# Kernel tuning notes

Measured on AMD Instinct MI355X. Metric: run time of the kernel, lower is better.

## Reference

```python
import jax, jax.numpy as jnp
import numpy as np

EPS_DEPTH = 0.001  # validity threshold from target_points.ge(0.001)
BIG = 1e10         # stands in for masked-out (padded) y points


def setup_inputs() -> dict:
    key = jax.random.key(0)
    k1, k2 = jax.random.split(key)
    L, N, P1 = 4, 4, 257          # n_scales, batch, n_bin_edges (256 bins)
    H, W = 240, 320
    bins = jax.random.uniform(k1, (L, N, P1), dtype=jnp.float32)
    target_depth_maps = jax.random.uniform(k2, (N, H, W), dtype=jnp.float32)
    return {"bins": bins, "target_depth_maps": target_depth_maps}


def _chamfer_1d(centers, y, mask, y_lengths):
    # centers: [N, P] bin centers; y: [N, M] flattened depths; mask: [N, M] valid
    # squared pairwise distances in 1-D: [N, P, M]
    d = (centers[:, :, None] - y[:, None, :]) ** 2
    # x -> y: min over VALID y points, mean over P bin centers
    dx = jnp.where(mask[:, None, :], d, BIG)
    cham_x = dx.min(axis=2).mean(axis=1)                       # [N]
    # y -> x: min over bin centers, sum over valid y / y_length
    dy = jnp.where(mask, d.min(axis=1), 0.0)                   # [N, M]
    cham_y = dy.sum(axis=1) / y_lengths                        # [N]
    return (cham_x + cham_y).mean()  # batch_reduction="mean"


def reference(bins, target_depth_maps):
    N = target_depth_maps.shape[0]
    y = target_depth_maps.reshape(N, -1)                       # [N, M]
    mask = y >= EPS_DEPTH                                      # ragged validity mask
    y_lengths = mask.sum(axis=1).astype(y.dtype)               # [N]
    loss = jnp.zeros((), dtype=y.dtype)
    for bin_edges in bins:  # fixed small loop over scales (multi=True)
        centers = 0.5 * (bin_edges[:, 1:] + bin_edges[:, :-1])  # [N, P]
        loss = loss + _chamfer_1d(centers, y, mask, y_lengths)
    return loss
```

## Files before the change

### kernel.cpp

```cpp
#include <hip/hip_runtime.h>


#define NSCALES 4
#define NBATCH  4
#define NEDGES  257
#define NP      256
#define NM      76800
#define CHUNK   512
#define NCHUNK  (NM / CHUNK)
#define BLOCK   256
#define NCENT   (NSCALES * NP)
#define BIGF    1e10f

__global__ __launch_bounds__(BLOCK) void bcl_init(float* __restrict__ minabs,
                                                  float* __restrict__ sumy,
                                                  unsigned int* __restrict__ cnt) {
    int t = blockIdx.x * blockDim.x + threadIdx.x;
    if (t < NSCALES * NBATCH * NP) minabs[t] = BIGF;
    if (t < NSCALES * NBATCH)      sumy[t]   = 0.0f;
    if (t < NBATCH)                cnt[t]    = 0u;
}

__global__ __launch_bounds__(BLOCK) void bcl_main(const float* __restrict__ bins,
                                                  const float* __restrict__ depth,
                                                  float* __restrict__ minabs,
                                                  float* __restrict__ sumy,
                                                  unsigned int* __restrict__ cnt) {
    __shared__ float sY[CHUNK];
    __shared__ float sC[NCENT];
    __shared__ float redS[BLOCK / 64][NSCALES];
    __shared__ unsigned int redC[BLOCK / 64];

    const int b = blockIdx.x;
    const int n = b / NCHUNK;
    const int chunk = b - n * NCHUNK;
    const int t = threadIdx.x;

    const float* yp = depth + n * NM + chunk * CHUNK;
#pragma unroll
    for (int k = 0; k < CHUNK / BLOCK; ++k) {
        float v = yp[t + k * BLOCK];
        sY[t + k * BLOCK] = (v >= 0.001f) ? v : 3e9f;
    }
#pragma unroll
    for (int k = 0; k < NCENT / BLOCK; ++k) {
        int i = t + k * BLOCK;
        int l = i >> 8;
        int p = i & (NP - 1);
        const float* be = bins + (l * NBATCH + n) * NEDGES + p;
        sC[i] = 0.5f * (be[0] + be[1]);
    }
    __syncthreads();

    float ca[NSCALES], ma[NSCALES];
#pragma unroll
    for (int k = 0; k < NSCALES; ++k) { ca[k] = sC[t + k * BLOCK]; ma[k] = BIGF; }

    const float4* sY4 = (const float4*)sY;
#pragma unroll 2
    for (int q = 0; q < CHUNK / 4; ++q) {
        float4 yv = sY4[q];
#pragma unroll
        for (int k = 0; k < NSCALES; ++k) {
            ma[k] = fminf(ma[k], fabsf(ca[k] - yv.x));
            ma[k] = fminf(ma[k], fabsf(ca[k] - yv.y));
            ma[k] = fminf(ma[k], fabsf(ca[k] - yv.z));
            ma[k] = fminf(ma[k], fabsf(ca[k] - yv.w));
        }
    }
#pragma unroll
    for (int k = 0; k < NSCALES; ++k)
        atomicMin((int*)(minabs + (k * NBATCH + n) * NP + t), __float_as_int(ma[k]));

    float yb0 = sY[t];
    float yb1 = sY[t + BLOCK];
    const bool v0 = yb0 < 2.0f, v1 = yb1 < 2.0f;

    float suml[NSCALES];
    const float4* sC4 = (const float4*)sC;
#pragma unroll
    for (int l = 0; l < NSCALES; ++l) {
        float m0 = BIGF, m1 = BIGF;
#pragma unroll 4
        for (int q = 0; q < NP / 4; ++q) {
            float4 c = sC4[l * (NP / 4) + q];
            m0 = fminf(m0, fabsf(c.x - yb0));  m1 = fminf(m1, fabsf(c.x - yb1));
            m0 = fminf(m0, fabsf(c.y - yb0));  m1 = fminf(m1, fabsf(c.y - yb1));
            m0 = fminf(m0, fabsf(c.z - yb0));  m1 = fminf(m1, fabsf(c.z - yb1));
            m0 = fminf(m0, fabsf(c.w - yb0));  m1 = fminf(m1, fabsf(c.w - yb1));
        }
        float s = 0.0f;
        if (v0) s += m0 * m0;
        if (v1) s += m1 * m1;
        suml[l] = s;
    }
    unsigned int c = (v0 ? 1u : 0u) + (v1 ? 1u : 0u);

#pragma unroll
    for (int off = 32; off; off >>= 1) {
#pragma unroll
        for (int l = 0; l < NSCALES; ++l) suml[l] += __shfl_down(suml[l], off);
        c += __shfl_down(c, off);
    }
    const int wv = t >> 6;
    if ((t & 63) == 0) {
#pragma unroll
        for (int l = 0; l < NSCALES; ++l) redS[wv][l] = suml[l];
        redC[wv] = c;
    }
    __syncthreads();
    if (t < NSCALES) {
        float s = redS[0][t] + redS[1][t] + redS[2][t] + redS[3][t];
        atomicAdd(&sumy[t * NBATCH + n], s);
    }
    if (t == 0) {
        unsigned int cc = redC[0] + redC[1] + redC[2] + redC[3];
        atomicAdd(&cnt[n], cc);
    }
}

__global__ __launch_bounds__(BLOCK) void bcl_final(const float* __restrict__ minabs,
                                                   const float* __restrict__ sumy,
                                                   const unsigned int* __restrict__ cnt,
                                                   float* __restrict__ out) {
    __shared__ float red[BLOCK / 64];
    int t = threadIdx.x;
    float s = 0.0f;
#pragma unroll
    for (int k = 0; k < (NSCALES * NBATCH * NP) / BLOCK; ++k) {
        float m = minabs[t + k * BLOCK];
        s += m * m;
    }
#pragma unroll
    for (int off = 32; off; off >>= 1) s += __shfl_down(s, off);
    if ((t & 63) == 0) red[t >> 6] = s;
    __syncthreads();
    if (t == 0) {
        float S = red[0] + red[1] + red[2] + red[3];
        float lossA = S / (float)NP;
        float lossB = 0.0f;
#pragma unroll
        for (int i = 0; i < NSCALES * NBATCH; ++i)
            lossB += sumy[i] / (float)cnt[i & (NBATCH - 1)];
        out[0] = (lossA + lossB) / (float)NBATCH;
    }
}

extern "C" void kernel_launch(void* const* d_in, const int* in_sizes, int n_in,
                              void* d_out, int out_size, void* d_ws, size_t ws_size,
                              hipStream_t stream) {
    const float* bins  = (const float*)d_in[0];
    const float* depth = (const float*)d_in[1];

    float* minabs = (float*)d_ws;
    float* sumy   = minabs + NSCALES * NBATCH * NP;
    unsigned int* cnt = (unsigned int*)(sumy + NSCALES * NBATCH);

    bcl_init<<<(NSCALES * NBATCH * NP + BLOCK - 1) / BLOCK, BLOCK, 0, stream>>>(minabs, sumy, cnt);
    bcl_main<<<NBATCH * NCHUNK, BLOCK, 0, stream>>>(bins, depth, minabs, sumy, cnt);
    bcl_final<<<1, BLOCK, 0, stream>>>(minabs, sumy, cnt, (float*)d_out);
}
```

Measured before the change: 85.35 us.

## Replace brute-force 1-D chamfer with sorted centers, binary search and interval extrema

A prep kernel computes the bin centers and sorts them with a bitonic sort per (scale, batch). The main kernel then binary-searches each depth value into the sorted centers to get its nearest-center distance. It also records per-interval max and min depth with shared-then-global atomics, so the x->y nearest depth can be recovered in the final kernel by prefix and suffix scans. This removes the O(P*M) brute-force min loops. In exchange it adds a sort, divergent searches and many atomics.

```diff
diff --git a/kernel.cpp b/kernel.cpp
--- a/kernel.cpp
+++ b/kernel.cpp
@@ -9,25 +9,59 @@
 #define CHUNK   512
 #define NCHUNK  (NM / CHUNK)
 #define BLOCK   256
-#define NCENT   (NSCALES * NP)
+#define NLN     (NSCALES * NBATCH)
+#define NIV     (NP + 1)
 #define BIGF    1e10f
-
-__global__ __launch_bounds__(BLOCK) void bcl_init(float* __restrict__ minabs,
-                                                  float* __restrict__ sumy,
-                                                  unsigned int* __restrict__ cnt) {
-    int t = blockIdx.x * blockDim.x + threadIdx.x;
-    if (t < NSCALES * NBATCH * NP) minabs[t] = BIGF;
-    if (t < NSCALES * NBATCH)      sumy[t]   = 0.0f;
-    if (t < NBATCH)                cnt[t]    = 0u;
-}
-
-__global__ __launch_bounds__(BLOCK) void bcl_main(const float* __restrict__ bins,
-                                                  const float* __restrict__ depth,
-                                                  float* __restrict__ minabs,
-                                                  float* __restrict__ sumy,
-                                                  unsigned int* __restrict__ cnt) {
-    __shared__ float sY[CHUNK];
-    __shared__ float sC[NCENT];
+#define IMIN    ((int)0x80000000)
+#define IMAX    0x7fffffff
+
+#define WS_SORTC 0
+#define WS_GA    (WS_SORTC + NLN * NP)
+#define WS_GB    (WS_GA + NLN * NIV)
+#define WS_SUMY  (WS_GB + NLN * NIV)
+#define WS_CNT   (WS_SUMY + NLN)
+
+__global__ __launch_bounds__(BLOCK) void bcl_prep(const float* __restrict__ bins,
+                                                  float* __restrict__ ws) {
+    __shared__ float s[NP];
+    const int b = blockIdx.x;
+    const int t = threadIdx.x;
+    const float* e = bins + b * NEDGES;
+    s[t] = 0.5f * (e[t] + e[t + 1]);
+
+    for (int k = 2; k <= NP; k <<= 1) {
+        for (int j = k >> 1; j > 0; j >>= 1) {
+            __syncthreads();
+            const int ixj = t ^ j;
+            const float a = s[t];
+            const float c = s[ixj];
+            const bool up = ((t & k) == 0);
+            float keep;
+            if (ixj > t) keep = up ? fminf(a, c) : fmaxf(a, c);
+            else         keep = up ? fmaxf(a, c) : fminf(a, c);
+            __syncthreads();
+            s[t] = keep;
+        }
+    }
+    __syncthreads();
+    ws[WS_SORTC + b * NP + t] = s[t];
+
+    int* gA = (int*)ws + WS_GA + b * NIV;
+    int* gB = (int*)ws + WS_GB + b * NIV;
+    gA[t] = IMIN;
+    gB[t] = IMAX;
+    if (t == 0) { gA[NP] = IMIN; gB[NP] = IMAX; }
+    if (b == 0) {
+        if (t < NLN)    ws[WS_SUMY + t] = 0.0f;
+        if (t < NBATCH) ((unsigned int*)ws)[WS_CNT + t] = 0u;
+    }
+}
+
+__global__ __launch_bounds__(BLOCK) void bcl_main(const float* __restrict__ depth,
+                                                  float* __restrict__ ws) {
+    __shared__ float sC[NSCALES * NP];
+    __shared__ int sA[NSCALES * NIV];
+    __shared__ int sB[NSCALES * NIV];
     __shared__ float redS[BLOCK / 64][NSCALES];
     __shared__ unsigned int redC[BLOCK / 64];
 
@@ -36,113 +70,134 @@
     const int chunk = b - n * NCHUNK;
     const int t = threadIdx.x;
 
+#pragma unroll
+    for (int l = 0; l < NSCALES; ++l)
+        sC[l * NP + t] = ws[WS_SORTC + (l * NBATCH + n) * NP + t];
+#pragma unroll
+    for (int i = t; i < NSCALES * NIV; i += BLOCK) { sA[i] = IMIN; sB[i] = IMAX; }
+
     const float* yp = depth + n * NM + chunk * CHUNK;
-#pragma unroll
-    for (int k = 0; k < CHUNK / BLOCK; ++k) {
-        float v = yp[t + k * BLOCK];
-        sY[t + k * BLOCK] = (v >= 0.001f) ? v : 3e9f;
-    }
-#pragma unroll
-    for (int k = 0; k < NCENT / BLOCK; ++k) {
-        int i = t + k * BLOCK;
-        int l = i >> 8;
-        int p = i & (NP - 1);
-        const float* be = bins + (l * NBATCH + n) * NEDGES + p;
-        sC[i] = 0.5f * (be[0] + be[1]);
-    }
-    __syncthreads();
-
-    float ca[NSCALES], ma[NSCALES];
-#pragma unroll
-    for (int k = 0; k < NSCALES; ++k) { ca[k] = sC[t + k * BLOCK]; ma[k] = BIGF; }
-
-    const float4* sY4 = (const float4*)sY;
-#pragma unroll 2
-    for (int q = 0; q < CHUNK / 4; ++q) {
-        float4 yv = sY4[q];
-#pragma unroll
-        for (int k = 0; k < NSCALES; ++k) {
-            ma[k] = fminf(ma[k], fabsf(ca[k] - yv.x));
-            ma[k] = fminf(ma[k], fabsf(ca[k] - yv.y));
-            ma[k] = fminf(ma[k], fabsf(ca[k] - yv.z));
-            ma[k] = fminf(ma[k], fabsf(ca[k] - yv.w));
+    const float y0 = yp[t];
+    const float y1 = yp[t + BLOCK];
+    const bool v0 = (y0 >= 0.001f);
+    const bool v1 = (y1 >= 0.001f);
+
+    __syncthreads();
+
+    float suml[NSCALES];
+#pragma unroll
+    for (int l = 0; l < NSCALES; ++l) suml[l] = 0.0f;
+
+#pragma unroll
+    for (int which = 0; which < 2; ++which) {
+        const float y = which ? y1 : y0;
+        const bool vv = which ? v1 : v0;
+        const int yb = __float_as_int(y);
+#pragma unroll
+        for (int l = 0; l < NSCALES; ++l) {
+            const float* c = sC + l * NP;
+            int j = -1;
+#pragma unroll
+            for (int step = NP; step; step >>= 1) {
+                const int cand = j + step;
+                const float v = c[cand < NP ? cand : NP - 1];
+                j = (cand < NP && v <= y) ? cand : j;
+            }
+            const float cb = c[j >= 0 ? j : 0];
+            const float ca = c[j + 1 < NP ? j + 1 : NP - 1];
+            const float dl = (j >= 0)      ? (y - cb) : BIGF;
+            const float dr = (j < NP - 1)  ? (ca - y) : BIGF;
+            const float d = fminf(dl, dr);
+            if (vv) {
+                suml[l] += d * d;
+                atomicMax(&sA[l * NIV + j + 1], yb);
+                atomicMin(&sB[l * NIV + j + 1], yb);
+            }
         }
     }
-#pragma unroll
-    for (int k = 0; k < NSCALES; ++k)
-        atomicMin((int*)(minabs + (k * NBATCH + n) * NP + t), __float_as_int(ma[k]));
-
-    float yb0 = sY[t];
-    float yb1 = sY[t + BLOCK];
-    const bool v0 = yb0 < 2.0f, v1 = yb1 < 2.0f;
-
-    float suml[NSCALES];
-    const float4* sC4 = (const float4*)sC;
+
+    __syncthreads();
+
+    int* gA = (int*)ws + WS_GA;
+    int* gB = (int*)ws + WS_GB;
 #pragma unroll
     for (int l = 0; l < NSCALES; ++l) {
-        float m0 = BIGF, m1 = BIGF;
-#pragma unroll 4
-        for (int q = 0; q < NP / 4; ++q) {
-            float4 c = sC4[l * (NP / 4) + q];
-            m0 = fminf(m0, fabsf(c.x - yb0));  m1 = fminf(m1, fabsf(c.x - yb1));
-            m0 = fminf(m0, fabsf(c.y - yb0));  m1 = fminf(m1, fabsf(c.y - yb1));
-            m0 = fminf(m0, fabsf(c.z - yb0));  m1 = fminf(m1, fabsf(c.z - yb1));
-            m0 = fminf(m0, fabsf(c.w - yb0));  m1 = fminf(m1, fabsf(c.w - yb1));
+        const int gbase = (l * NBATCH + n) * NIV;
+        for (int k = t; k < NIV; k += BLOCK) {
+            const int a = sA[l * NIV + k];
+            if (a != IMIN && a > gA[gbase + k]) atomicMax(&gA[gbase + k], a);
+            const int bb = sB[l * NIV + k];
+            if (bb != IMAX && bb < gB[gbase + k]) atomicMin(&gB[gbase + k], bb);
         }
-        float s = 0.0f;
-        if (v0) s += m0 * m0;
-        if (v1) s += m1 * m1;
-        suml[l] = s;
-    }
-    unsigned int c = (v0 ? 1u : 0u) + (v1 ? 1u : 0u);
-
+    }
+
+    unsigned int cc = (v0 ? 1u : 0u) + (v1 ? 1u : 0u);
 #pragma unroll
     for (int off = 32; off; off >>= 1) {
 #pragma unroll
         for (int l = 0; l < NSCALES; ++l) suml[l] += __shfl_down(suml[l], off);
-        c += __shfl_down(c, off);
+        cc += __shfl_down(cc, off);
     }
     const int wv = t >> 6;
     if ((t & 63) == 0) {
 #pragma unroll
         for (int l = 0; l < NSCALES; ++l) redS[wv][l] = suml[l];
-        redC[wv] = c;
+        redC[wv] = cc;
     }
     __syncthreads();
     if (t < NSCALES) {
-        float s = redS[0][t] + redS[1][t] + redS[2][t] + redS[3][t];
-        atomicAdd(&sumy[t * NBATCH + n], s);
+        const float s2 = redS[0][t] + redS[1][t] + redS[2][t] + redS[3][t];
+        atomicAdd(&ws[WS_SUMY + t * NBATCH + n], s2);
     }
     if (t == 0) {
-        unsigned int cc = redC[0] + redC[1] + redC[2] + redC[3];
-        atomicAdd(&cnt[n], cc);
-    }
-}
-
-__global__ __launch_bounds__(BLOCK) void bcl_final(const float* __restrict__ minabs,
-                                                   const float* __restrict__ sumy,
-                                                   const unsigned int* __restrict__ cnt,
+        const unsigned int c4 = redC[0] + redC[1] + redC[2] + redC[3];
+        atomicAdd(&((unsigned int*)ws)[WS_CNT + n], c4);
+    }
+}
+
+__global__ __launch_bounds__(BLOCK) void bcl_final(const float* __restrict__ wsf,
                                                    float* __restrict__ out) {
+    __shared__ int lA[NLN * NIV];
+    __shared__ int lB[NLN * NIV];
     __shared__ float red[BLOCK / 64];
-    int t = threadIdx.x;
-    float s = 0.0f;
-#pragma unroll
-    for (int k = 0; k < (NSCALES * NBATCH * NP) / BLOCK; ++k) {
-        float m = minabs[t + k * BLOCK];
-        s += m * m;
-    }
-#pragma unroll
-    for (int off = 32; off; off >>= 1) s += __shfl_down(s, off);
-    if ((t & 63) == 0) red[t >> 6] = s;
+    const int t = threadIdx.x;
+    const int* gA = (const int*)wsf + WS_GA;
+    const int* gB = (const int*)wsf + WS_GB;
+    for (int i = t; i < NLN * NIV; i += BLOCK) { lA[i] = gA[i]; lB[i] = gB[i]; }
+    __syncthreads();
+
+    if (t < NLN) {
+        const int base = t * NIV;
+        int run = IMIN;
+        for (int k = 0; k < NP; ++k) { run = max(run, lA[base + k]); lA[base + k] = run; }
+        int run2 = IMAX;
+        for (int p = NP - 1; p >= 0; --p) { run2 = min(run2, lB[base + p + 1]); lB[base + p + 1] = run2; }
+    }
+    __syncthreads();
+
+    float tot = 0.0f;
+#pragma unroll
+    for (int ln = 0; ln < NLN; ++ln) {
+        const float c = wsf[WS_SORTC + ln * NP + t];
+        const int fl = lA[ln * NIV + t];
+        const int fr = lB[ln * NIV + t + 1];
+        const float dl = (fl == IMIN) ? BIGF : (c - __int_as_float(fl));
+        const float dr = (fr == IMAX) ? BIGF : (__int_as_float(fr) - c);
+        const float m = fminf(dl, dr);
+        tot += m * m;
+    }
+#pragma unroll
+    for (int off = 32; off; off >>= 1) tot += __shfl_down(tot, off);
+    if ((t & 63) == 0) red[t >> 6] = tot;
     __syncthreads();
     if (t == 0) {
-        float S = red[0] + red[1] + red[2] + red[3];
-        float lossA = S / (float)NP;
+        const float S = red[0] + red[1] + red[2] + red[3];
         float lossB = 0.0f;
 #pragma unroll
-        for (int i = 0; i < NSCALES * NBATCH; ++i)
-            lossB += sumy[i] / (float)cnt[i & (NBATCH - 1)];
-        out[0] = (lossA + lossB) / (float)NBATCH;
+        for (int i = 0; i < NLN; ++i)
+            lossB += wsf[WS_SUMY + i] /
+                     (float)((const unsigned int*)wsf)[WS_CNT + (i & (NBATCH - 1))];
+        out[0] = (S / (float)NP + lossB) / (float)NBATCH;
     }
 }
 
@@ -151,12 +206,9 @@
                               hipStream_t stream) {
     const float* bins  = (const float*)d_in[0];
     const float* depth = (const float*)d_in[1];
-
-    float* minabs = (float*)d_ws;
-    float* sumy   = minabs + NSCALES * NBATCH * NP;
-    unsigned int* cnt = (unsigned int*)(sumy + NSCALES * NBATCH);
-
-    bcl_init<<<(NSCALES * NBATCH * NP + BLOCK - 1) / BLOCK, BLOCK, 0, stream>>>(minabs, sumy, cnt);
-    bcl_main<<<NBATCH * NCHUNK, BLOCK, 0, stream>>>(bins, depth, minabs, sumy, cnt);
-    bcl_final<<<1, BLOCK, 0, stream>>>(minabs, sumy, cnt, (float*)d_out);
-}
+    float* ws = (float*)d_ws;
+
+    bcl_prep <<<NLN,           BLOCK, 0, stream>>>(bins, ws);
+    bcl_main <<<NBATCH*NCHUNK, BLOCK, 0, stream>>>(depth, ws);
+    bcl_final<<<1,             BLOCK, 0, stream>>>(ws, (float*)d_out);
+}
```

New measurement: 120.5 us. +41.2%, slower.
